# Performance work log

Hardware: AMD Instinct MI355X
Metric: run time of the kernel (lower is better)

Reference implementation:

```python
import jax, jax.numpy as jnp
import numpy as np

K_CLUSTERS = 512
N_ITERS = 10  # fixed Lloyd iterations (torch_kmeans uses max_iter with tol; fixed count keeps it jit-friendly)


def setup_inputs() -> dict:
    key = jax.random.key(0)
    x = jax.random.normal(key, (4, 8192, 256), dtype=jnp.float32)  # (B, N, D)
    return {"x": x}


def _sq_dists(x, centers):
    # x: (B,N,D), centers: (B,K,D) -> squared Euclidean distances (B,N,K)
    xc = jnp.einsum('bnd,bkd->bnk', x, centers)
    x2 = jnp.sum(x * x, axis=-1, keepdims=True)          # (B,N,1)
    c2 = jnp.sum(centers * centers, axis=-1)[:, None, :]  # (B,1,K)
    return x2 - 2.0 * xc + c2


def _kmeans(x, k=K_CLUSTERS, iters=N_ITERS):
    # deterministic init: first k points of each batch as initial centroids
    centers0 = x[:, :k, :]  # (B,K,D)

    def step(centers, _):
        labels = jnp.argmin(_sq_dists(x, centers), axis=-1)          # (B,N)
        onehot = jax.nn.one_hot(labels, k, dtype=x.dtype)            # (B,N,K)
        sums = jnp.einsum('bnk,bnd->bkd', onehot, x)                 # (B,K,D)
        counts = jnp.sum(onehot, axis=1)                             # (B,K)
        new_centers = jnp.where(
            counts[..., None] > 0,
            sums / jnp.maximum(counts, 1.0)[..., None],
            centers,  # keep empty clusters' previous centroid
        )
        return new_centers, None

    centers, _ = jax.lax.scan(step, centers0, None, length=iters)
    labels = jnp.argmin(_sq_dists(x, centers), axis=-1)
    return labels, centers


def reference(x):
    labels, centers = _kmeans(x)
    return labels, centers
```

## Files before the change

kernel.cpp:

```cpp
#include <hip/hip_runtime.h>
#include <math.h>

#define BB 4
#define NN 8192
#define DD 256
#define KK 512
#define NITERS 10

#define TAU 0.06f
#define NCH 128

typedef _Float16 f16;
typedef f16   f16x8 __attribute__((ext_vector_type(8)));
typedef float f32x4 __attribute__((ext_vector_type(4)));

__global__ __launch_bounds__(256) void init_centers_k(const float* __restrict__ x,
                                                      float* __restrict__ centers,
                                                      f16* __restrict__ chh,
                                                      float* __restrict__ c2) {
    __shared__ float sq[256];
    int bk = blockIdx.x;
    int b  = bk >> 9;
    int k  = bk & 511;
    int t  = threadIdx.x;
    size_t idx = (size_t)bk * DD + t;
    float v = x[((size_t)b * NN + k) * DD + t];
    centers[idx] = v;
    chh[idx] = (f16)v;
    sq[t] = v * v;
    __syncthreads();
    for (int s = 128; s > 0; s >>= 1) {
        if (t < s) sq[t] += sq[t + s];
        __syncthreads();
    }
    if (t == 0) c2[bk] = sq[0];
}

__global__ __launch_bounds__(256) void xsplit_k(const float* __restrict__ x,
                                                f16* __restrict__ xh,
                                                f16* __restrict__ xl) {
    size_t i = ((size_t)blockIdx.x * 256 + threadIdx.x) * 8;
    float4 a  = *(const float4*)(x + i);
    float4 bq = *(const float4*)(x + i + 4);
    float vf[8] = {a.x, a.y, a.z, a.w, bq.x, bq.y, bq.z, bq.w};
    f16x8 hv, lv;
    #pragma unroll
    for (int j = 0; j < 8; ++j) {
        f16 h = (f16)vf[j];
        hv[j] = h;
        lv[j] = (f16)(vf[j] - (float)h);
    }
    *(f16x8*)(xh + i) = hv;
    *(f16x8*)(xl + i) = lv;
}

__global__ __launch_bounds__(256) void rowsumsq_k(const float* __restrict__ rows,
                                                  float* __restrict__ out, int nrows) {
    int r = blockIdx.x * 256 + threadIdx.x;
    if (r >= nrows) return;
    const float* p = rows + (size_t)r * DD;
    float total = 0.f;
    #pragma unroll
    for (int h = 0; h < 2; ++h) {
        float a[8];
        #pragma unroll
        for (int j = 0; j < 8; ++j) a[j] = 0.f;
        for (int i = 0; i < 128; i += 8) {
            #pragma unroll
            for (int j = 0; j < 8; ++j) {
                float v  = p[h * 128 + i + j];
                float sq = __fmul_rn(v, v);
                a[j] = __fadd_rn(a[j], sq);
            }
        }
        float s = __fadd_rn(__fadd_rn(__fadd_rn(a[0], a[1]), __fadd_rn(a[2], a[3])),
                            __fadd_rn(__fadd_rn(a[4], a[5]), __fadd_rn(a[6], a[7])));
        total = __fadd_rn(total, s);
    }
    out[r] = total;
}

__global__ __launch_bounds__(256, 2) void assign_k(
    const f16* __restrict__ xh, const f16* __restrict__ xl,
    const f16* __restrict__ chh,
    const float* __restrict__ x2g, const float* __restrict__ c2g,
    int* __restrict__ labels, int* __restrict__ flagslot, int* __restrict__ flaglist)
{
    __shared__ f16 xlh[64 * 256];
    __shared__ f16 xll[64 * 256];
    __shared__ float rv1s[4][64];
    __shared__ float rv2s[4][64];
    __shared__ int   rk1s[4][64];

    const int tid  = threadIdx.x;
    const int wid  = tid >> 6;
    const int lane = tid & 63;
    const int l15  = lane & 15;
    const int lg   = lane >> 4;
    const int b    = blockIdx.x >> 7;
    const int m0   = (blockIdx.x & 127) * 64;

    const f16* xhb = xh + (size_t)(b * NN + m0) * DD;
    const f16* xlb = xl + (size_t)(b * NN + m0) * DD;

    #pragma unroll
    for (int i = 0; i < 8; ++i) {
        int lin = tid + i * 256;
        int row = lin >> 5, g = lin & 31;
        size_t goff = (size_t)row * DD + g * 8;
        f16x8 hv = *(const f16x8*)(xhb + goff);
        f16x8 lv = *(const f16x8*)(xlb + goff);
        int si = row * 256 + ((g ^ (row & 7)) << 3);
        *(f16x8*)&xlh[si] = hv;
        *(f16x8*)&xll[si] = lv;
    }
    __syncthreads();

    const f16* bhb = chh + ((size_t)b * KK + wid * 128) * DD;

    f32x4 acc[4][8];
    #pragma unroll
    for (int mi = 0; mi < 4; ++mi)
        #pragma unroll
        for (int ki = 0; ki < 8; ++ki)
            acc[mi][ki] = (f32x4){0.f, 0.f, 0.f, 0.f};

    #pragma unroll
    for (int s = 0; s < 8; ++s) {
        const int d0 = s * 32;
        f16x8 bh[8];
        #pragma unroll
        for (int ki = 0; ki < 8; ++ki) {
            size_t off = (size_t)(ki * 16 + l15) * DD + d0 + lg * 8;
            bh[ki] = *(const f16x8*)(bhb + off);
        }
        f16x8 ah[4], al[4];
        #pragma unroll
        for (int mi = 0; mi < 4; ++mi) {
            int row = mi * 16 + l15;
            int g   = (d0 >> 3) + lg;
            int si  = row * 256 + ((g ^ (row & 7)) << 3);
            ah[mi] = *(const f16x8*)&xlh[si];
            al[mi] = *(const f16x8*)&xll[si];
        }
        #pragma unroll
        for (int ki = 0; ki < 8; ++ki) {
            #pragma unroll
            for (int mi = 0; mi < 4; ++mi) {
                acc[mi][ki] = __builtin_amdgcn_mfma_f32_16x16x32_f16(ah[mi], bh[ki], acc[mi][ki], 0, 0, 0);
                acc[mi][ki] = __builtin_amdgcn_mfma_f32_16x16x32_f16(al[mi], bh[ki], acc[mi][ki], 0, 0, 0);
            }
        }
    }

    float c2v[8];
    #pragma unroll
    for (int ki = 0; ki < 8; ++ki)
        c2v[ki] = c2g[b * KK + wid * 128 + ki * 16 + l15];

    #pragma unroll
    for (int mi = 0; mi < 4; ++mi) {
        #pragma unroll
        for (int r = 0; r < 4; ++r) {
            int p = mi * 16 + lg * 4 + r;
            float x2p = x2g[b * NN + m0 + p];
            float v1 = __builtin_inff(), v2 = __builtin_inff();
            int   k1 = 0x7fffffff;
            #pragma unroll
            for (int ki = 0; ki < 8; ++ki) {
                float s    = acc[mi][ki][r];
                float cand = __fadd_rn(__fsub_rn(x2p, __fmul_rn(2.0f, s)), c2v[ki]);
                int   kidx = wid * 128 + ki * 16 + l15;
                if (cand < v1 || (cand == v1 && kidx < k1)) { v2 = v1; v1 = cand; k1 = kidx; }
                else if (cand < v2) v2 = cand;
            }
            #pragma unroll
            for (int off = 1; off < 16; off <<= 1) {
                float ov1 = __shfl_xor(v1, off, 64);
                int   ok1 = __shfl_xor(k1, off, 64);
                float ov2 = __shfl_xor(v2, off, 64);
                if (ov1 < v1 || (ov1 == v1 && ok1 < k1)) { v2 = fminf(v1, ov2); v1 = ov1; k1 = ok1; }
                else v2 = fminf(v2, ov1);
            }
            if (l15 == 0) { rv1s[wid][p] = v1; rv2s[wid][p] = v2; rk1s[wid][p] = k1; }
        }
    }
    __syncthreads();
    if (tid < 64) {
        float v1 = rv1s[0][tid], v2 = rv2s[0][tid];
        int   k1 = rk1s[0][tid];
        #pragma unroll
        for (int w = 1; w < 4; ++w) {
            float ov1 = rv1s[w][tid], ov2 = rv2s[w][tid];
            int   ok1 = rk1s[w][tid];
            if (ov1 < v1 || (ov1 == v1 && ok1 < k1)) { v2 = fminf(v1, ov2); v1 = ov1; k1 = ok1; }
            else v2 = fminf(v2, ov1);
        }
        int g = b * NN + m0 + tid;
        labels[g] = k1;
        if (v2 - v1 < TAU) {
            int pos = atomicAdd(flagslot, 1);
            flaglist[pos] = g;
        }
    }
}

__global__ __launch_bounds__(256) void refine_k(const float* __restrict__ x,
                                                const float* __restrict__ centers,
                                                const int* __restrict__ flagslot,
                                                const int* __restrict__ flaglist,
                                                int* __restrict__ labels,
                                                int* __restrict__ dirty) {
    __shared__ float  xsr[DD];
    __shared__ double sv[256];
    __shared__ int    si[256];
    const int t = threadIdx.x;
    if (t < 2) dirty[blockIdx.x * 2 + t] = 0;
    const int cnt = flagslot[0];
    for (int idx = blockIdx.x; idx < cnt; idx += gridDim.x) {
        const int g = flaglist[idx];
        const int b = g >> 13;
        __syncthreads();
        xsr[t] = x[(size_t)g * DD + t];
        __syncthreads();
        const float* cbase = centers + (size_t)b * KK * DD;
        double bestv = 1e300; int bestk = 0x7fffffff;
        #pragma unroll
        for (int h = 0; h < 2; ++h) {
            int k = t + h * 256;
            const float* cr = cbase + (size_t)k * DD;
            double a0 = 0, a1 = 0, a2 = 0, a3 = 0;
            for (int d = 0; d < DD; d += 4) {
                float4 cv = *(const float4*)(cr + d);
                double f0 = (double)xsr[d + 0] - (double)cv.x;
                double f1 = (double)xsr[d + 1] - (double)cv.y;
                double f2 = (double)xsr[d + 2] - (double)cv.z;
                double f3 = (double)xsr[d + 3] - (double)cv.w;
                a0 += f0 * f0; a1 += f1 * f1; a2 += f2 * f2; a3 += f3 * f3;
            }
            double dist = (a0 + a1) + (a2 + a3);
            if (dist < bestv || (dist == bestv && k < bestk)) { bestv = dist; bestk = k; }
        }
        sv[t] = bestv; si[t] = bestk;
        __syncthreads();
        for (int s = 128; s > 0; s >>= 1) {
            if (t < s) {
                if (sv[t + s] < sv[t] || (sv[t + s] == sv[t] && si[t + s] < si[t])) {
                    sv[t] = sv[t + s]; si[t] = si[t + s];
                }
            }
            __syncthreads();
        }
        if (t == 0) labels[g] = si[0];
    }
}

__global__ __launch_bounds__(64) void chunk_hist_k(const int* __restrict__ labels,
                                                   int* __restrict__ labels_prev,
                                                   int* __restrict__ dirty,
                                                   int* __restrict__ chunkhist) {
    __shared__ int h[KK];
    const int bc = blockIdx.x;
    const int b  = bc >> 7;
    const int c  = bc & (NCH - 1);
    const int t  = threadIdx.x;
    for (int k = t; k < KK; k += 64) h[k] = 0;
    __syncthreads();
    int n  = b * NN + c * 64 + t;
    int l  = labels[n];
    int lp = labels_prev[n];
    atomicAdd(&h[l], 1);
    if (l != lp) {
        dirty[b * KK + l] = 1;
        if (lp >= 0 && lp < KK) dirty[b * KK + lp] = 1;
        labels_prev[n] = l;
    }
    __syncthreads();
    int* ch = chunkhist + (size_t)bc * KK;
    for (int k = t; k < KK; k += 64) ch[k] = h[k];
}

__global__ __launch_bounds__(512) void scan_k(int* __restrict__ chunkhist,
                                              int* __restrict__ counts,
                                              int* __restrict__ offsets) {
    __shared__ int s[KK];
    const int b = blockIdx.x;
    const int k = threadIdx.x;
    int* ch = chunkhist + (size_t)b * NCH * KK;
    int run = 0;
    for (int c0 = 0; c0 < NCH; c0 += 16) {
        int v[16];
        #pragma unroll
        for (int j = 0; j < 16; ++j) v[j] = ch[(size_t)(c0 + j) * KK + k];
        #pragma unroll
        for (int j = 0; j < 16; ++j) {
            ch[(size_t)(c0 + j) * KK + k] = run;
            run += v[j];
        }
    }
    counts[b * KK + k] = run;
    s[k] = run;
    __syncthreads();
    for (int off = 1; off < KK; off <<= 1) {
        int v = (k >= off) ? s[k - off] : 0;
        __syncthreads();
        s[k] += v;
        __syncthreads();
    }
    offsets[b * KK + k] = s[k] - run;
}

__global__ __launch_bounds__(64) void scatter_k(const int* __restrict__ labels,
                                                const int* __restrict__ chunkhist,
                                                const int* __restrict__ offsets,
                                                int* __restrict__ idxlist) {
    const int bc = blockIdx.x;
    const int b  = bc >> 7;
    const int c  = bc & (NCH - 1);
    const int t  = threadIdx.x;
    const int n  = c * 64 + t;
    const int l  = labels[b * NN + n];
    int rank = 0;
    for (int j = 0; j < 64; ++j) {
        int lj = __shfl(l, j, 64);
        rank += (lj == l && j < t) ? 1 : 0;
    }
    int base = offsets[b * KK + l] + chunkhist[(size_t)bc * KK + l];
    idxlist[b * NN + base + rank] = n;
}

__global__ __launch_bounds__(1024) void centers_update_k(const float* __restrict__ x,
                                                         float* __restrict__ centers,
                                                         f16* __restrict__ chh,
                                                         float* __restrict__ c2,
                                                         const int* __restrict__ counts,
                                                         const int* __restrict__ offsets,
                                                         const int* __restrict__ idxlist,
                                                         const int* __restrict__ dirty) {
    __shared__ float part[16][DD];
    __shared__ float sq[256];
    const int bk   = blockIdx.x;
    const int b    = bk >> 9;
    const int tid  = threadIdx.x;
    const int w    = tid >> 6;
    const int lane = tid & 63;
    if (!dirty[bk]) return;
    const int cnt = counts[bk];
    if (cnt == 0) return;
    const int* il = idxlist + b * NN + offsets[bk];
    const float* xb = x + (size_t)b * NN * DD;
    float4 acc = {0.f, 0.f, 0.f, 0.f};
    #pragma unroll 8
    for (int j = w; j < cnt; j += 16) {
        int n = il[j];
        float4 v = *(const float4*)(xb + (size_t)n * DD + lane * 4);
        acc.x = __fadd_rn(acc.x, v.x);
        acc.y = __fadd_rn(acc.y, v.y);
        acc.z = __fadd_rn(acc.z, v.z);
        acc.w = __fadd_rn(acc.w, v.w);
    }
    *(float4*)&part[w][lane * 4] = acc;
    __syncthreads();
    float val = 0.f;
    if (tid < DD) {
        float s = 0.f;
        #pragma unroll
        for (int w2 = 0; w2 < 16; ++w2) s = __fadd_rn(s, part[w2][tid]);
        val = s / (float)cnt;
        size_t idx = (size_t)bk * DD + tid;
        centers[idx] = val;
        chh[idx] = (f16)val;
    }
    if (tid < 256) sq[tid] = val * val;
    __syncthreads();
    for (int s = 128; s > 0; s >>= 1) {
        if (tid < s) sq[tid] += sq[tid + s];
        __syncthreads();
    }
    if (tid == 0) c2[bk] = sq[0];
}

__global__ __launch_bounds__(256) void out_k(const int* __restrict__ labels,
                                             const float* __restrict__ centers,
                                             float* __restrict__ out) {
    size_t i = (size_t)blockIdx.x * 256 + threadIdx.x;
    if (i < (size_t)BB * NN) out[i] = (float)labels[i];
    else                     out[i] = centers[i - (size_t)BB * NN];
}

extern "C" void kernel_launch(void* const* d_in, const int* in_sizes, int n_in,
                              void* d_out, int out_size, void* d_ws, size_t ws_size,
                              hipStream_t stream) {
    const float* x = (const float*)d_in[0];
    float* out = (float*)d_out;
    float* ws  = (float*)d_ws;

    float* centers  = ws;
    float* c2       = centers + (size_t)BB * KK * DD;
    float* x2       = c2 + BB * KK;
    int*   labels   = (int*)(x2 + BB * NN);
    int*   flagcnt  = labels + BB * NN;
    int*   flaglist = flagcnt + 64;
    int*   counts   = flaglist + BB * NN;
    int*   offsets  = counts + BB * KK;
    int*   idxlist  = offsets + BB * KK;
    int*   chunkhist= idxlist + BB * NN;
    f16*   chh      = (f16*)(chunkhist + (size_t)BB * NCH * KK);
    int*   labels_prev = (int*)(chh + (size_t)BB * KK * DD);
    int*   dirty    = labels_prev + BB * NN;
    f16*   xh16     = (f16*)(dirty + BB * KK);
    f16*   xl16     = xh16 + (size_t)BB * NN * DD;

    hipMemsetAsync(flagcnt, 0, 64 * sizeof(int), stream);
    hipMemsetAsync(labels_prev, 0xFF, (size_t)BB * NN * sizeof(int), stream);

    init_centers_k<<<BB * KK, 256, 0, stream>>>(x, centers, chh, c2);
    xsplit_k<<<(int)((size_t)BB * NN * DD / 8 / 256), 256, 0, stream>>>(x, xh16, xl16);
    rowsumsq_k<<<(BB * NN + 255) / 256, 256, 0, stream>>>(x, x2, BB * NN);

    for (int it = 0; it < NITERS; ++it) {
        assign_k<<<BB * (NN / 64), 256, 0, stream>>>(xh16, xl16, chh, x2, c2,
                                                     labels, flagcnt + it, flaglist);
        refine_k<<<1024, 256, 0, stream>>>(x, centers, flagcnt + it, flaglist,
                                           labels, dirty);
        chunk_hist_k<<<BB * NCH, 64, 0, stream>>>(labels, labels_prev, dirty, chunkhist);
        scan_k<<<BB, 512, 0, stream>>>(chunkhist, counts, offsets);
        scatter_k<<<BB * NCH, 64, 0, stream>>>(labels, chunkhist, offsets, idxlist);
        centers_update_k<<<BB * KK, 1024, 0, stream>>>(x, centers, chh, c2,
                                                       counts, offsets, idxlist, dirty);
    }

    assign_k<<<BB * (NN / 64), 256, 0, stream>>>(xh16, xl16, chh, x2, c2,
                                                 labels, flagcnt + NITERS, flaglist);
    refine_k<<<1024, 256, 0, stream>>>(x, centers, flagcnt + NITERS, flaglist,
                                       labels, dirty);

    out_k<<<(int)(((size_t)BB * NN + (size_t)BB * KK * DD + 255) / 256), 256, 0, stream>>>(
        labels, centers, out);
}
```

Before: 945.4 us.

## Replace histogram/scan/scatter index build with per-cluster label scan in center update

Removes the chunk histogram, prefix-scan and scatter kernels that built a per-cluster index list. Instead, each center-update block scans all labels of its batch and accumulates the points whose label matches its cluster, counting them on the fly. This cuts kernel launches and intermediate buffers per iteration. In exchange, every dirty cluster block now reads the full label array, a quadratic amount of label traffic with a serial branchy loop.

```diff
diff --git a/kernel.cpp b/kernel.cpp
--- a/kernel.cpp
+++ b/kernel.cpp
@@ -8,7 +8,6 @@
 #define NITERS 10
 
 #define TAU 0.06f
-#define NCH 128
 
 typedef _Float16 f16;
 typedef f16   f16x8 __attribute__((ext_vector_type(8)));
@@ -255,118 +254,70 @@
     }
 }
 
-__global__ __launch_bounds__(64) void chunk_hist_k(const int* __restrict__ labels,
-                                                   int* __restrict__ labels_prev,
-                                                   int* __restrict__ dirty,
-                                                   int* __restrict__ chunkhist) {
-    __shared__ int h[KK];
-    const int bc = blockIdx.x;
-    const int b  = bc >> 7;
-    const int c  = bc & (NCH - 1);
-    const int t  = threadIdx.x;
-    for (int k = t; k < KK; k += 64) h[k] = 0;
-    __syncthreads();
-    int n  = b * NN + c * 64 + t;
+__global__ __launch_bounds__(256) void dirty_k(const int* __restrict__ labels,
+                                               int* __restrict__ labels_prev,
+                                               int* __restrict__ dirty) {
+    int n = blockIdx.x * 256 + threadIdx.x;
+    int b = n >> 13;
     int l  = labels[n];
     int lp = labels_prev[n];
-    atomicAdd(&h[l], 1);
     if (l != lp) {
         dirty[b * KK + l] = 1;
         if (lp >= 0 && lp < KK) dirty[b * KK + lp] = 1;
         labels_prev[n] = l;
     }
-    __syncthreads();
-    int* ch = chunkhist + (size_t)bc * KK;
-    for (int k = t; k < KK; k += 64) ch[k] = h[k];
-}
-
-__global__ __launch_bounds__(512) void scan_k(int* __restrict__ chunkhist,
-                                              int* __restrict__ counts,
-                                              int* __restrict__ offsets) {
-    __shared__ int s[KK];
-    const int b = blockIdx.x;
-    const int k = threadIdx.x;
-    int* ch = chunkhist + (size_t)b * NCH * KK;
-    int run = 0;
-    for (int c0 = 0; c0 < NCH; c0 += 16) {
-        int v[16];
-        #pragma unroll
-        for (int j = 0; j < 16; ++j) v[j] = ch[(size_t)(c0 + j) * KK + k];
-        #pragma unroll
-        for (int j = 0; j < 16; ++j) {
-            ch[(size_t)(c0 + j) * KK + k] = run;
-            run += v[j];
-        }
-    }
-    counts[b * KK + k] = run;
-    s[k] = run;
-    __syncthreads();
-    for (int off = 1; off < KK; off <<= 1) {
-        int v = (k >= off) ? s[k - off] : 0;
-        __syncthreads();
-        s[k] += v;
-        __syncthreads();
-    }
-    offsets[b * KK + k] = s[k] - run;
-}
-
-__global__ __launch_bounds__(64) void scatter_k(const int* __restrict__ labels,
-                                                const int* __restrict__ chunkhist,
-                                                const int* __restrict__ offsets,
-                                                int* __restrict__ idxlist) {
-    const int bc = blockIdx.x;
-    const int b  = bc >> 7;
-    const int c  = bc & (NCH - 1);
-    const int t  = threadIdx.x;
-    const int n  = c * 64 + t;
-    const int l  = labels[b * NN + n];
-    int rank = 0;
-    for (int j = 0; j < 64; ++j) {
-        int lj = __shfl(l, j, 64);
-        rank += (lj == l && j < t) ? 1 : 0;
-    }
-    int base = offsets[b * KK + l] + chunkhist[(size_t)bc * KK + l];
-    idxlist[b * NN + base + rank] = n;
 }
 
 __global__ __launch_bounds__(1024) void centers_update_k(const float* __restrict__ x,
+                                                         const int* __restrict__ labels,
                                                          float* __restrict__ centers,
                                                          f16* __restrict__ chh,
                                                          float* __restrict__ c2,
-                                                         const int* __restrict__ counts,
-                                                         const int* __restrict__ offsets,
-                                                         const int* __restrict__ idxlist,
                                                          const int* __restrict__ dirty) {
     __shared__ float part[16][DD];
+    __shared__ int   cnts[16];
     __shared__ float sq[256];
     const int bk   = blockIdx.x;
     const int b    = bk >> 9;
+    const int k    = bk & 511;
     const int tid  = threadIdx.x;
     const int w    = tid >> 6;
     const int lane = tid & 63;
     if (!dirty[bk]) return;
-    const int cnt = counts[bk];
-    if (cnt == 0) return;
-    const int* il = idxlist + b * NN + offsets[bk];
+    const int* lb = labels + b * NN;
     const float* xb = x + (size_t)b * NN * DD;
     float4 acc = {0.f, 0.f, 0.f, 0.f};
-    #pragma unroll 8
-    for (int j = w; j < cnt; j += 16) {
-        int n = il[j];
-        float4 v = *(const float4*)(xb + (size_t)n * DD + lane * 4);
-        acc.x = __fadd_rn(acc.x, v.x);
-        acc.y = __fadd_rn(acc.y, v.y);
-        acc.z = __fadd_rn(acc.z, v.z);
-        acc.w = __fadd_rn(acc.w, v.w);
+    int cnt = 0;
+    #pragma unroll 4
+    for (int n = w * 512; n < (w + 1) * 512; ++n) {
+        if (lb[n] == k) {
+            float4 v = *(const float4*)(xb + (size_t)n * DD + lane * 4);
+            acc.x = __fadd_rn(acc.x, v.x);
+            acc.y = __fadd_rn(acc.y, v.y);
+            acc.z = __fadd_rn(acc.z, v.z);
+            acc.w = __fadd_rn(acc.w, v.w);
+            ++cnt;
+        }
     }
     *(float4*)&part[w][lane * 4] = acc;
-    __syncthreads();
+    if (lane == 0) cnts[w] = cnt;
+    __syncthreads();
+    __shared__ int total;
+    if (tid == 0) {
+        int s = 0;
+        #pragma unroll
+        for (int w2 = 0; w2 < 16; ++w2) s += cnts[w2];
+        total = s;
+    }
+    __syncthreads();
+    const int tc = total;
+    if (tc == 0) return;
     float val = 0.f;
     if (tid < DD) {
         float s = 0.f;
         #pragma unroll
         for (int w2 = 0; w2 < 16; ++w2) s = __fadd_rn(s, part[w2][tid]);
-        val = s / (float)cnt;
+        val = s / (float)tc;
         size_t idx = (size_t)bk * DD + tid;
         centers[idx] = val;
         chh[idx] = (f16)val;
@@ -401,14 +352,10 @@
     int*   labels   = (int*)(x2 + BB * NN);
     int*   flagcnt  = labels + BB * NN;
     int*   flaglist = flagcnt + 64;
-    int*   counts   = flaglist + BB * NN;
-    int*   offsets  = counts + BB * KK;
-    int*   idxlist  = offsets + BB * KK;
-    int*   chunkhist= idxlist + BB * NN;
-    f16*   chh      = (f16*)(chunkhist + (size_t)BB * NCH * KK);
-    int*   labels_prev = (int*)(chh + (size_t)BB * KK * DD);
+    int*   labels_prev = flaglist + BB * NN;
     int*   dirty    = labels_prev + BB * NN;
-    f16*   xh16     = (f16*)(dirty + BB * KK);
+    f16*   chh      = (f16*)(dirty + BB * KK);
+    f16*   xh16     = chh + (size_t)BB * KK * DD;
     f16*   xl16     = xh16 + (size_t)BB * NN * DD;
 
     hipMemsetAsync(flagcnt, 0, 64 * sizeof(int), stream);
@@ -423,11 +370,9 @@
                                                      labels, flagcnt + it, flaglist);
         refine_k<<<1024, 256, 0, stream>>>(x, centers, flagcnt + it, flaglist,
                                            labels, dirty);
-        chunk_hist_k<<<BB * NCH, 64, 0, stream>>>(labels, labels_prev, dirty, chunkhist);
-        scan_k<<<BB, 512, 0, stream>>>(chunkhist, counts, offsets);
-        scatter_k<<<BB * NCH, 64, 0, stream>>>(labels, chunkhist, offsets, idxlist);
-        centers_update_k<<<BB * KK, 1024, 0, stream>>>(x, centers, chh, c2,
-                                                       counts, offsets, idxlist, dirty);
+        dirty_k<<<BB * NN / 256, 256, 0, stream>>>(labels, labels_prev, dirty);
+        centers_update_k<<<BB * KK, 1024, 0, stream>>>(x, labels, centers, chh, c2,
+                                                       dirty);
     }
 
     assign_k<<<BB * (NN / 64), 256, 0, stream>>>(xh16, xl16, chh, x2, c2,
```

Measured after the change: 1.813 ms. +91.7%, slower.
